# Kernel tuning notes

Hardware: AMD Instinct MI355X
Metric: run time of the kernel (lower is better)

Reference implementation:

```python
import jax, jax.numpy as jnp
import numpy as np
from itertools import product


def _gen_exps(num_vars, degree):
    return [e for e in product(range(degree + 1), repeat=num_vars) if sum(e) <= degree]

EXP_W = _gen_exps(7, 3)  # 120 terms
EXP_B = _gen_exps(3, 3)  # 20 terms
EXP_M = _gen_exps(5, 3)  # 56 terms (+1 diagonal coeff)


def _powers(x, exps):
    return {e: x ** e for e in exps}


def setup_inputs() -> dict:
    key = jax.random.key(0)
    ks = jax.random.split(key, 12)
    B, Din, Dout = 65536, 64, 64
    return {
        'x1': jax.random.normal(ks[0], (B, Din), jnp.float32),
        's1': jax.random.normal(ks[1], (B, Dout), jnp.float32),
        'y1': jax.random.normal(ks[2], (B, Dout), jnp.float32),
        'x2': jax.random.normal(ks[3], (B, Din), jnp.float32),
        's2': jax.random.normal(ks[4], (B, Dout), jnp.float32),
        'y2': jax.random.normal(ks[5], (B, Dout), jnp.float32),
        'w': jax.random.normal(ks[6], (Dout, Din), jnp.float32) * 0.1,
        'b': jax.random.normal(ks[7], (Dout,), jnp.float32) * 0.1,
        'm': jax.random.normal(ks[8], (Dout, Dout), jnp.float32) * 0.1,
        'params_w': jax.random.normal(ks[9], (len(EXP_W),), jnp.float32) * 0.1,
        'params_b': jax.random.normal(ks[10], (len(EXP_B),), jnp.float32) * 0.1,
        'params_m': jax.random.normal(ks[11], (len(EXP_M) + 1,), jnp.float32) * 0.1,
    }


def _dw(x1, s1, y1, x2, s2, y2, w, params_w):
    px1 = _powers(x1, {e[0] for e in EXP_W})
    ps1 = _powers(s1, {e[1] for e in EXP_W})
    py1 = _powers(y1, {e[2] for e in EXP_W})
    px2 = _powers(x2, {e[3] for e in EXP_W})
    ps2 = _powers(s2, {e[4] for e in EXP_W})
    py2 = _powers(y2, {e[5] for e in EXP_W})
    pw = _powers(w, {e[6] for e in EXP_W})
    inv_b = 1.0 / x1.shape[0]
    delta_w = jnp.zeros_like(w)
    for i, e in enumerate(EXP_W):
        y_term = ps1[e[1]] * py1[e[2]] * ps2[e[4]] * py2[e[5]]  # [B, Dout]
        x_term = px1[e[0]] * px2[e[3]]                          # [B, Din]
        delta_w = delta_w + (params_w[i] * inv_b) * (y_term.T @ x_term) * pw[e[6]]
    return delta_w  # bound=None (identity), l2_reg=0


def _db(y1, y2, b, params_b):
    py1 = _powers(y1, {e[0] for e in EXP_B})
    py2 = _powers(y2, {e[1] for e in EXP_B})
    pb = _powers(b, {e[2] for e in EXP_B})
    inv_b = 1.0 / y1.shape[0]
    delta_b = jnp.zeros_like(b)
    for i, e in enumerate(EXP_B):
        delta_b = delta_b + (params_b[i] * inv_b) * jnp.sum(py1[e[0]] * py2[e[1]], axis=0) * pb[e[2]]
    return delta_b


def _dm(y1, y2, m, params_m):
    ey1 = {e[0] for e in EXP_M} | {e[1] for e in EXP_M}
    ey2 = {e[2] for e in EXP_M} | {e[3] for e in EXP_M}
    py1 = _powers(y1, ey1)
    py2 = _powers(y2, ey2)
    pm = _powers(m, {e[4] for e in EXP_M})
    inv_b = 1.0 / y1.shape[0]
    delta_m = jnp.zeros_like(m)
    for i, e in enumerate(EXP_M):
        left = py1[e[1]] * py2[e[3]]   # [B, Dout]
        right = py1[e[0]] * py2[e[2]]  # [B, Dout]
        delta_m = delta_m + (params_m[i] * inv_b) * (left.T @ right) * pm[e[4]]
    delta_m = delta_m + params_m[-1] * jnp.eye(m.shape[0], dtype=m.dtype)
    return delta_m


def reference(x1, s1, y1, x2, s2, y2, w, b, m, params_w, params_b, params_m):
    delta_w = _dw(x1, s1, y1, x2, s2, y2, w, params_w)
    delta_b = _db(y1, y2, b, params_b)
    delta_m = _dm(y1, y2, m, params_m)
    return delta_w, delta_b, delta_m
```

## Files before the change

kernel.cpp:

```cpp
#include <hip/hip_runtime.h>
#include <type_traits>
#include <stdint.h>

#define DEV __device__ __forceinline__

typedef float f32x4 __attribute__((ext_vector_type(4)));
typedef short bf16x8 __attribute__((ext_vector_type(8)));
typedef unsigned short u16;
typedef u16 u16x4 __attribute__((ext_vector_type(4)));

static constexpr int BTOT = 65536;
static constexpr int KB   = 64;
static constexpr int NCHT = BTOT / KB;
static constexpr int NG   = 56;
static constexpr int NCOLSUM = 45;
static constexpr float INVB = 1.0f / (float)BTOT;

static constexpr int NBLK_M  = 24;
static constexpr int NBLK_W1 = 48;
static constexpr int NBLK_W2 = 48;
static constexpr int NBLK_W3 = 64;
static constexpr int NBLK_R  = 328;
static constexpr int GRID    = NBLK_M+NBLK_W1+NBLK_W2+NBLK_W3+NBLK_R;
static constexpr int THR_M  = NBLK_M;
static constexpr int THR_W1 = THR_M + NBLK_W1;
static constexpr int THR_W2 = THR_W1 + NBLK_W2;
static constexpr int THR_W3 = THR_W2 + NBLK_W3;

struct Col {
  int nslot, np, nsplit, nb;
  int8_t sexp[10][6];
  int8_t pa[16], pb[16];
  int16_t gout[16];
  uint8_t ldmask;
};

struct Tables {
  int nW, nB, nM, nA, nX;
  int8_t expw[120][7];
  int8_t expb[20][3];
  int8_t expm[56][5];
  int8_t am[35][4];
  int8_t xm[10][2];
  Col col[4];
  int8_t wtype[120]; int16_t widx[120]; int8_t wpow[120];
  int8_t mtype[56];  int16_t midx[56];  int8_t mpow[56];
  int16_t bcol[20];  int8_t bpow[20];
  int err, gcount;
};

constexpr int aidf(const Tables& t,int a,int b,int c,int d){
  for(int i=0;i<t.nA;i++)
    if(t.am[i][0]==a&&t.am[i][1]==b&&t.am[i][2]==c&&t.am[i][3]==d) return i;
  return -1;
}
constexpr int xidf(const Tables& t,int a,int b){
  for(int i=0;i<t.nX;i++) if(t.xm[i][0]==a&&t.xm[i][1]==b) return i;
  return -1;
}

constexpr Tables makeTables(){
  Tables t{};
  t.err = 0;
  t.nW=0;
  for(int e0=0;e0<4;e0++)for(int e1=0;e1<4;e1++)for(int e2=0;e2<4;e2++)
  for(int e3=0;e3<4;e3++)for(int e4=0;e4<4;e4++)for(int e5=0;e5<4;e5++)
  for(int e6=0;e6<4;e6++) if(e0+e1+e2+e3+e4+e5+e6<=3){
    t.expw[t.nW][0]=(int8_t)e0; t.expw[t.nW][1]=(int8_t)e1; t.expw[t.nW][2]=(int8_t)e2;
    t.expw[t.nW][3]=(int8_t)e3; t.expw[t.nW][4]=(int8_t)e4; t.expw[t.nW][5]=(int8_t)e5;
    t.expw[t.nW][6]=(int8_t)e6; t.nW++;
  }
  t.nB=0;
  for(int e0=0;e0<4;e0++)for(int e1=0;e1<4;e1++)for(int e2=0;e2<4;e2++)
    if(e0+e1+e2<=3){ t.expb[t.nB][0]=(int8_t)e0; t.expb[t.nB][1]=(int8_t)e1; t.expb[t.nB][2]=(int8_t)e2; t.nB++; }
  t.nM=0;
  for(int e0=0;e0<4;e0++)for(int e1=0;e1<4;e1++)for(int e2=0;e2<4;e2++)
  for(int e3=0;e3<4;e3++)for(int e4=0;e4<4;e4++)
    if(e0+e1+e2+e3+e4<=3){
      t.expm[t.nM][0]=(int8_t)e0; t.expm[t.nM][1]=(int8_t)e1; t.expm[t.nM][2]=(int8_t)e2;
      t.expm[t.nM][3]=(int8_t)e3; t.expm[t.nM][4]=(int8_t)e4; t.nM++;
    }
  t.nA=0;
  for(int a=0;a<4;a++)for(int b=0;b<4;b++)for(int c=0;c<4;c++)for(int d=0;d<4;d++)
    if(a+b+c+d<=3){ t.am[t.nA][0]=(int8_t)a; t.am[t.nA][1]=(int8_t)b; t.am[t.nA][2]=(int8_t)c; t.am[t.nA][3]=(int8_t)d; t.nA++; }
  t.nX=0;
  for(int a=0;a<4;a++)for(int b=0;b<4;b++)
    if(a+b<=3){ t.xm[t.nX][0]=(int8_t)a; t.xm[t.nX][1]=(int8_t)b; t.nX++; }

  int wslot[35][10]; int mslot[10][10];
  for(int i=0;i<35;i++)for(int j=0;j<10;j++) wslot[i][j]=-1;
  for(int i=0;i<10;i++)for(int j=0;j<10;j++) mslot[i][j]=-1;

  int slot=0;

  {
    Col& c = t.col[0]; c.nslot=5; c.nsplit=1; c.nb=NBLK_M;
    int ye[5][2] = {{0,1},{1,0},{0,2},{1,1},{2,0}};
    int xmid[5] = {0,0,0,0,0};
    for(int s=0;s<5;s++){
      c.sexp[s][0]=0; c.sexp[s][1]=(int8_t)ye[s][0]; c.sexp[s][2]=0;
      c.sexp[s][3]=(int8_t)ye[s][1]; c.sexp[s][4]=0; c.sexp[s][5]=0;
      xmid[s]=xidf(t, ye[s][0], ye[s][1]);
      if(xmid[s]<0) t.err+=1;
    }
    int p=0;
    for(int L=0;L<2;L++)for(int R=0;R<5;R++){
      c.pa[p]=(int8_t)L; c.pb[p]=(int8_t)R; c.gout[p]=(int16_t)slot;
      mslot[xmid[L]][xmid[R]]=slot; slot++; p++;
    }
    for(int L=2;L<5;L++)for(int R=0;R<2;R++){
      c.pa[p]=(int8_t)L; c.pb[p]=(int8_t)R; c.gout[p]=(int16_t)slot;
      mslot[xmid[L]][xmid[R]]=slot; slot++; p++;
    }
    c.np=p;
    if(p!=16) t.err+=1;
  }
  for(int wc=0; wc<2; wc++){
    Col& c = t.col[1+wc]; c.nslot=10; c.nsplit=1; c.nb = wc? NBLK_W2 : NBLK_W1;
    int ae[5][2] = {{1,0},{0,1},{2,0},{1,1},{0,2}};
    int xe[5][2] = {{0,1},{1,0},{0,2},{1,1},{2,0}};
    int amid[5]={0,0,0,0,0}, xmidb[5]={0,0,0,0,0};
    for(int s=0;s<5;s++){
      for(int q=0;q<6;q++) c.sexp[s][q]=0;
      if(wc==0){ c.sexp[s][0]=(int8_t)ae[s][0]; c.sexp[s][1]=(int8_t)ae[s][1];
                 amid[s]=aidf(t, ae[s][0], ae[s][1], 0, 0); }
      else     { c.sexp[s][2]=(int8_t)ae[s][0]; c.sexp[s][3]=(int8_t)ae[s][1];
                 amid[s]=aidf(t, 0, 0, ae[s][0], ae[s][1]); }
      if(amid[s]<0) t.err+=1;
      for(int q=0;q<6;q++) c.sexp[5+s][q]=0;
      c.sexp[5+s][4]=(int8_t)xe[s][0]; c.sexp[5+s][5]=(int8_t)xe[s][1];
      xmidb[s]=xidf(t, xe[s][0], xe[s][1]);
      if(xmidb[s]<0) t.err+=1;
    }
    int p=0;
    for(int a=0;a<2;a++)for(int b=0;b<5;b++){
      c.pa[p]=(int8_t)a; c.pb[p]=(int8_t)(5+b); c.gout[p]=(int16_t)slot;
      wslot[amid[a]][xmidb[b]]=slot; slot++; p++;
    }
    for(int a=2;a<5;a++)for(int b=0;b<2;b++){
      c.pa[p]=(int8_t)a; c.pb[p]=(int8_t)(5+b); c.gout[p]=(int16_t)slot;
      wslot[amid[a]][xmidb[b]]=slot; slot++; p++;
    }
    c.np=p;
    if(p!=16) t.err+=1;
  }
  {
    Col& c = t.col[3]; c.nslot=6; c.nsplit=2; c.nb=NBLK_W3;
    int ae4[4][4] = {{1,0,1,0},{1,0,0,1},{0,1,1,0},{0,1,0,1}};
    int xe[2][2] = {{0,1},{1,0}};
    int amid[4]={0,0,0,0}, xmidb[2]={0,0};
    for(int s=0;s<4;s++){
      c.sexp[s][0]=(int8_t)ae4[s][0]; c.sexp[s][1]=(int8_t)ae4[s][1];
      c.sexp[s][2]=(int8_t)ae4[s][2]; c.sexp[s][3]=(int8_t)ae4[s][3];
      c.sexp[s][4]=0; c.sexp[s][5]=0;
      amid[s]=aidf(t, ae4[s][0], ae4[s][1], ae4[s][2], ae4[s][3]);
      if(amid[s]<0) t.err+=1;
    }
    for(int s=0;s<2;s++){
      for(int q=0;q<6;q++) c.sexp[4+s][q]=0;
      c.sexp[4+s][4]=(int8_t)xe[s][0]; c.sexp[4+s][5]=(int8_t)xe[s][1];
      xmidb[s]=xidf(t, xe[s][0], xe[s][1]);
      if(xmidb[s]<0) t.err+=1;
    }
    int p=0;
    for(int a=0;a<4;a++)for(int b=0;b<2;b++){
      c.pa[p]=(int8_t)a; c.pb[p]=(int8_t)(4+b); c.gout[p]=(int16_t)slot;
      wslot[amid[a]][xmidb[b]]=slot; slot++; p++;
    }
    c.np=p;
    if(p!=8) t.err+=1;
  }
  t.gcount=slot;
  if(slot!=NG) t.err+=1;

  for(int ci=0; ci<4; ci++){
    unsigned m=0;
    for(int s=0;s<t.col[ci].nslot;s++)
      for(int v=0;v<6;v++) if(t.col[ci].sexp[s][v]>0) m |= (1u<<v);
    t.col[ci].ldmask=(uint8_t)m;
  }

  for(int i=0;i<t.nW;i++){
    const int8_t* e=t.expw[i];
    bool u0=(e[0]==0&&e[3]==0);
    bool v0=(e[1]==0&&e[2]==0&&e[4]==0&&e[5]==0);
    t.wpow[i]=e[6];
    if(u0){ t.wtype[i]=1; t.widx[i]=(int16_t)aidf(t,e[1],e[2],e[4],e[5]); }
    else if(v0){ t.wtype[i]=2; t.widx[i]=(int16_t)xidf(t,e[0],e[3]); }
    else {
      int s=wslot[aidf(t,e[1],e[2],e[4],e[5])][xidf(t,e[0],e[3])];
      if(s<0) t.err+=1;
      t.wtype[i]=0; t.widx[i]=(int16_t)s;
    }
  }
  for(int i=0;i<t.nM;i++){
    const int8_t* e=t.expm[i];
    bool L0=(e[1]==0&&e[3]==0), R0=(e[0]==0&&e[2]==0);
    t.mpow[i]=e[4];
    if(L0){ t.mtype[i]=2; t.midx[i]=(int16_t)aidf(t,0,e[0],0,e[2]); }
    else if(R0){ t.mtype[i]=1; t.midx[i]=(int16_t)aidf(t,0,e[1],0,e[3]); }
    else {
      int s=mslot[xidf(t,e[1],e[3])][xidf(t,e[0],e[2])];
      if(s<0) t.err+=1;
      t.mtype[i]=0; t.midx[i]=(int16_t)s;
    }
  }
  for(int i=0;i<t.nB;i++){
    const int8_t* e=t.expb[i];
    t.bcol[i]=(int16_t)aidf(t,0,e[0],0,e[1]); t.bpow[i]=e[2];
  }
  return t;
}

constexpr Tables TB = makeTables();
static_assert(TB.err==0 && TB.gcount==56, "table build failed");
static_assert(TB.nW==120 && TB.nB==20 && TB.nM==56 && TB.nA==35 && TB.nX==10, "enumeration mismatch");

template<int N, typename F>
DEV void sunroll(F&& f){
  if constexpr (N > 0){
    sunroll<N-1>(static_cast<F&&>(f));
    f(std::integral_constant<int, N-1>{});
  }
}
template<int E> DEV float ipw(float x){
  if constexpr(E==0) return 1.0f;
  else if constexpr(E==1) return x;
  else if constexpr(E==2) return x*x;
  else return x*x*x;
}
DEV u16 f2bf(float f){
  uint32_t u = __builtin_bit_cast(uint32_t, f);
  u = u + 0x7FFFu + ((u>>16)&1u);
  return (u16)(u>>16);
}

DEV bf16x8 readFrag(const u16* lds, int slot, int sb, int t, int l){
  const int base = slot*4096 + ((sb*2 + ((l>>4)>>1))*256 + t*64 + ((l>>4)&1)*32 + (l&15))*4;
  const u16x4 lo = *(const u16x4*)&lds[base];
  const u16x4 hi = *(const u16x4*)&lds[base + 64];
  bf16x8 r;
  r[0]=(short)lo[0]; r[1]=(short)lo[1]; r[2]=(short)lo[2]; r[3]=(short)lo[3];
  r[4]=(short)hi[0]; r[5]=(short)hi[1]; r[6]=(short)hi[2]; r[7]=(short)hi[3];
  return r;
}

template<int CI>
DEV void colGemm(const float* __restrict__ s1,const float* __restrict__ y1,
                 const float* __restrict__ s2,const float* __restrict__ y2,
                 const float* __restrict__ x1,const float* __restrict__ x2,
                 float* __restrict__ G, u16* lds, int tid, int bi)
{
  constexpr int NS  = TB.col[CI].nslot;
  constexpr int NSP = TB.col[CI].nsplit;
  constexpr int NDB = 4/NSP;
  constexpr int NB  = TB.col[CI].nb;
  constexpr unsigned LM = TB.col[CI].ldmask;

  const int l=tid&63, ob=(tid>>6)&3, sub=tid>>8, w=tid>>6;
  const int ch = ob*16 + (l&15);
  const int bl = sub*16 + ((l>>4)&3)*4;

  int aslot=0,bslot=0,gsl=0,dbase=0;
  sunroll<16>([&](auto W){
    constexpr int ww = decltype(W)::value;
    if(w==ww){
      constexpr int p = ww/NSP;
      aslot = TB.col[CI].pa[p];
      bslot = TB.col[CI].pb[p];
      gsl   = TB.col[CI].gout[p];
      dbase = (ww%NSP)*2;
    }
  });

  const int c0 = (bi*NCHT)/NB, c1 = ((bi+1)*NCHT)/NB;
  f32x4 acc[4][NDB] = {};

  float raw[6][4] = {};
  float nraw[6][4] = {};

  auto issue = [&](int ck, float (&dst)[6][4]){
    const int b0 = (ck*KB + bl)*64 + ch;
    #pragma unroll
    for(int j=0;j<4;j++){
      const int off = b0 + j*64;
      if constexpr(LM&1u)  dst[0][j]=s1[off];
      if constexpr(LM&2u)  dst[1][j]=y1[off];
      if constexpr(LM&4u)  dst[2][j]=s2[off];
      if constexpr(LM&8u)  dst[3][j]=y2[off];
      if constexpr(LM&16u) dst[4][j]=x1[off];
      if constexpr(LM&32u) dst[5][j]=x2[off];
    }
  };

  issue(c0, raw);

  for(int ck=c0; ck<c1; ++ck){
    const int nk = (ck+1<c1)? ck+1 : c0;
    issue(nk, nraw);

    sunroll<NS>([&](auto S){
      constexpr int s = decltype(S)::value;
      u16x4 o4;
      #pragma unroll
      for(int j=0;j<4;j++){
        float v = ipw<TB.col[CI].sexp[s][0]>(raw[0][j])
                * ipw<TB.col[CI].sexp[s][1]>(raw[1][j])
                * ipw<TB.col[CI].sexp[s][2]>(raw[2][j])
                * ipw<TB.col[CI].sexp[s][3]>(raw[3][j])
                * ipw<TB.col[CI].sexp[s][4]>(raw[4][j])
                * ipw<TB.col[CI].sexp[s][5]>(raw[5][j]);
        o4[j]=f2bf(v);
      }
      *(u16x4*)&lds[s*4096 + tid*4] = o4;
    });

    asm volatile("s_waitcnt lgkmcnt(0)" ::: "memory");
    __builtin_amdgcn_s_barrier();
    __builtin_amdgcn_sched_barrier(0);

    #pragma unroll
    for(int sb=0; sb<2; ++sb){
      bf16x8 Af[4];
      #pragma unroll
      for(int o2=0;o2<4;o2++) Af[o2]=readFrag(lds,aslot,sb,o2,l);
      #pragma unroll
      for(int dd=0;dd<NDB;dd++){
        bf16x8 Bf=readFrag(lds,bslot,sb,dbase+dd,l);
        #pragma unroll
        for(int o2=0;o2<4;o2++)
          acc[o2][dd]=__builtin_amdgcn_mfma_f32_16x16x32_bf16(Af[o2],Bf,acc[o2][dd],0,0,0);
      }
    }

    __builtin_amdgcn_sched_barrier(0);
    __builtin_amdgcn_s_barrier();
    __builtin_amdgcn_sched_barrier(0);

    #pragma unroll
    for(int a=0;a<6;a++)
      #pragma unroll
      for(int j=0;j<4;j++) raw[a][j]=nraw[a][j];
  }

  float* dst = G + gsl*4096;
  const int r0=(l>>4)*4, cc=l&15;
  #pragma unroll
  for(int o2=0;o2<4;o2++)
    #pragma unroll
    for(int dd=0;dd<NDB;dd++)
      #pragma unroll
      for(int r=0;r<4;r++)
        atomicAdd(&dst[(o2*16+r0+r)*64 + (dbase+dd)*16+cc], acc[o2][dd][r]);
}

DEV void colRed(const float* __restrict__ s1,const float* __restrict__ y1,
                const float* __restrict__ s2,const float* __restrict__ y2,
                const float* __restrict__ x1,const float* __restrict__ x2,
                float* __restrict__ col, float* ldsF, int tid, int bi)
{
  const int ch=tid&63, g=tid>>6;
  const int c0=(bi*NCHT)/NBLK_R, c1=((bi+1)*NCHT)/NBLK_R;
  float accv[45];
  sunroll<45>([&](auto K){ accv[decltype(K)::value]=0.f; });
  for(int r=c0*KB+g; r<c1*KB; r+=16){
    const int off=r*64+ch;
    const float v0=s1[off],v1=y1[off],v2=s2[off],v3=y2[off],v4=x1[off],v5=x2[off];
    sunroll<35>([&](auto K){
      constexpr int k=decltype(K)::value;
      accv[k] += ipw<TB.am[k][0]>(v0)*ipw<TB.am[k][1]>(v1)*ipw<TB.am[k][2]>(v2)*ipw<TB.am[k][3]>(v3);
    });
    sunroll<10>([&](auto K){
      constexpr int k=decltype(K)::value;
      accv[35+k] += ipw<TB.xm[k][0]>(v4)*ipw<TB.xm[k][1]>(v5);
    });
  }
  sunroll<5>([&](auto RR){
    constexpr int rr=decltype(RR)::value;
    __syncthreads();
    sunroll<9>([&](auto Q){
      constexpr int q=decltype(Q)::value;
      ldsF[(q*16+g)*64+ch]=accv[rr*9+q];
    });
    __syncthreads();
    if(tid<576){
      const int q=tid>>6, c=tid&63;
      float s=0.f;
      #pragma unroll
      for(int gg=0; gg<16; gg++) s+=ldsF[(q*16+gg)*64+c];
      atomicAdd(&col[(rr*9+q)*64+c], s);
    }
  });
}

__global__ __launch_bounds__(1024) void k_main(
    const float* __restrict__ x1, const float* __restrict__ s1, const float* __restrict__ y1,
    const float* __restrict__ x2, const float* __restrict__ s2, const float* __restrict__ y2,
    float* __restrict__ G, float* __restrict__ col)
{
  __shared__ u16 lds[10*4096];
  const int tid = threadIdx.x;
  const int bx = blockIdx.x;
  if      (bx < THR_M)  colGemm<0>(s1,y1,s2,y2,x1,x2,G,lds,tid,bx);
  else if (bx < THR_W1) colGemm<1>(s1,y1,s2,y2,x1,x2,G,lds,tid,bx-THR_M);
  else if (bx < THR_W2) colGemm<2>(s1,y1,s2,y2,x1,x2,G,lds,tid,bx-THR_W1);
  else if (bx < THR_W3) colGemm<3>(s1,y1,s2,y2,x1,x2,G,lds,tid,bx-THR_W2);
  else                  colRed(s1,y1,s2,y2,x1,x2,col,(float*)lds,tid,bx-THR_W3);
}

__global__ __launch_bounds__(256) void k_combine(
    const float* __restrict__ G, const float* __restrict__ col,
    const float* __restrict__ w, const float* __restrict__ b, const float* __restrict__ m,
    const float* __restrict__ parw, const float* __restrict__ parb, const float* __restrict__ parm,
    float* __restrict__ out)
{
  const int n = blockIdx.x*256 + threadIdx.x;
  const int o = n>>6, d = n&63;
  const float wv = w[n], mv = m[n];
  const float wp[4] = {1.f, wv, wv*wv, wv*wv*wv};
  const float mp[4] = {1.f, mv, mv*mv, mv*mv*mv};
  float aw=0.f, am=0.f;
  sunroll<120>([&](auto II){
    constexpr int i = decltype(II)::value;
    constexpr int ty = TB.wtype[i];
    constexpr int ix = TB.widx[i];
    constexpr int q  = TB.wpow[i];
    float val;
    if constexpr(ty==0) val = G[ix*4096 + n];
    else if constexpr(ty==1) val = col[ix*64 + o];
    else val = col[(35+ix)*64 + d];
    aw += parw[i] * val * wp[q];
  });
  sunroll<56>([&](auto II){
    constexpr int i = decltype(II)::value;
    constexpr int ty = TB.mtype[i];
    constexpr int ix = TB.midx[i];
    constexpr int q  = TB.mpow[i];
    float val;
    if constexpr(ty==0) val = G[ix*4096 + n];
    else if constexpr(ty==1) val = col[ix*64 + o];
    else val = col[ix*64 + d];
    am += parm[i] * val * mp[q];
  });
  aw *= INVB; am *= INVB;
  if (o==d) am += parm[56];
  out[n] = aw;
  out[4160 + n] = am;
  if (n < 64){
    const float bv = b[n];
    const float bp[4] = {1.f, bv, bv*bv, bv*bv*bv};
    float ab=0.f;
    sunroll<20>([&](auto II){
      constexpr int i = decltype(II)::value;
      constexpr int cix = TB.bcol[i];
      constexpr int q = TB.bpow[i];
      ab += parb[i] * col[cix*64 + n] * bp[q];
    });
    out[4096 + n] = ab * INVB;
  }
}

extern "C" void kernel_launch(void* const* d_in, const int* in_sizes, int n_in,
                              void* d_out, int out_size, void* d_ws, size_t ws_size,
                              hipStream_t stream)
{
  const float* x1=(const float*)d_in[0];
  const float* s1=(const float*)d_in[1];
  const float* y1=(const float*)d_in[2];
  const float* x2=(const float*)d_in[3];
  const float* s2=(const float*)d_in[4];
  const float* y2=(const float*)d_in[5];
  const float* w =(const float*)d_in[6];
  const float* b =(const float*)d_in[7];
  const float* m =(const float*)d_in[8];
  const float* parw=(const float*)d_in[9];
  const float* parb=(const float*)d_in[10];
  const float* parm=(const float*)d_in[11];

  float* G   = (float*)d_ws;
  float* col = G + NG*4096;

  hipMemsetAsync(d_ws, 0, (size_t)(NG*4096 + NCOLSUM*64)*sizeof(float), stream);
  k_main<<<GRID, 1024, 0, stream>>>(x1,s1,y1,x2,s2,y2,G,col);
  k_combine<<<16, 256, 0, stream>>>(G,col,w,b,m,parw,parb,parm,(float*)d_out);
}
```

Before: 103.6 us.

## Store LDS in MFMA fragment order and rebalance grid into uniform windows

Each thread now writes its bf16 values into LDS at positions that already match the MFMA fragment layout. Fragment reads become a single 16-byte load instead of two 8-byte loads plus a repack. The grid is also rebalanced: every GEMM column type gets 64 blocks and the reduction gets 256 blocks, indexed by window. This changes how work is split across CUs and how chunks are spread. The new write pattern may cause LDS bank conflicts on the store side.

```diff
diff --git a/kernel.cpp b/kernel.cpp
--- a/kernel.cpp
+++ b/kernel.cpp
@@ -16,16 +16,10 @@
 static constexpr int NCOLSUM = 45;
 static constexpr float INVB = 1.0f / (float)BTOT;
 
-static constexpr int NBLK_M  = 24;
-static constexpr int NBLK_W1 = 48;
-static constexpr int NBLK_W2 = 48;
-static constexpr int NBLK_W3 = 64;
-static constexpr int NBLK_R  = 328;
-static constexpr int GRID    = NBLK_M+NBLK_W1+NBLK_W2+NBLK_W3+NBLK_R;
-static constexpr int THR_M  = NBLK_M;
-static constexpr int THR_W1 = THR_M + NBLK_W1;
-static constexpr int THR_W2 = THR_W1 + NBLK_W2;
-static constexpr int THR_W3 = THR_W2 + NBLK_W3;
+static constexpr int NWIN   = 64;
+static constexpr int NBLK_C = 64;
+static constexpr int NBLK_R = 256;
+static constexpr int GRID   = 8*NWIN;
 
 struct Col {
   int nslot, np, nsplit, nb;
@@ -94,7 +88,7 @@
   int slot=0;
 
   {
-    Col& c = t.col[0]; c.nslot=5; c.nsplit=1; c.nb=NBLK_M;
+    Col& c = t.col[0]; c.nslot=5; c.nsplit=1; c.nb=NBLK_C;
     int ye[5][2] = {{0,1},{1,0},{0,2},{1,1},{2,0}};
     int xmid[5] = {0,0,0,0,0};
     for(int s=0;s<5;s++){
@@ -116,7 +110,7 @@
     if(p!=16) t.err+=1;
   }
   for(int wc=0; wc<2; wc++){
-    Col& c = t.col[1+wc]; c.nslot=10; c.nsplit=1; c.nb = wc? NBLK_W2 : NBLK_W1;
+    Col& c = t.col[1+wc]; c.nslot=10; c.nsplit=1; c.nb=NBLK_C;
     int ae[5][2] = {{1,0},{0,1},{2,0},{1,1},{0,2}};
     int xe[5][2] = {{0,1},{1,0},{0,2},{1,1},{2,0}};
     int amid[5]={0,0,0,0,0}, xmidb[5]={0,0,0,0,0};
@@ -145,7 +139,7 @@
     if(p!=16) t.err+=1;
   }
   {
-    Col& c = t.col[3]; c.nslot=6; c.nsplit=2; c.nb=NBLK_W3;
+    Col& c = t.col[3]; c.nslot=6; c.nsplit=2; c.nb=NBLK_C;
     int ae4[4][4] = {{1,0,1,0},{1,0,0,1},{0,1,1,0},{0,1,0,1}};
     int xe[2][2] = {{0,1},{1,0}};
     int amid[4]={0,0,0,0}, xmidb[2]={0,0};
@@ -236,13 +230,7 @@
 }
 
 DEV bf16x8 readFrag(const u16* lds, int slot, int sb, int t, int l){
-  const int base = slot*4096 + ((sb*2 + ((l>>4)>>1))*256 + t*64 + ((l>>4)&1)*32 + (l&15))*4;
-  const u16x4 lo = *(const u16x4*)&lds[base];
-  const u16x4 hi = *(const u16x4*)&lds[base + 64];
-  bf16x8 r;
-  r[0]=(short)lo[0]; r[1]=(short)lo[1]; r[2]=(short)lo[2]; r[3]=(short)lo[3];
-  r[4]=(short)hi[0]; r[5]=(short)hi[1]; r[6]=(short)hi[2]; r[7]=(short)hi[3];
-  return r;
+  return *(const bf16x8*)&lds[slot*4096 + ((sb*4 + t)*64 + l)*8];
 }
 
 template<int CI>
@@ -258,8 +246,10 @@
   constexpr unsigned LM = TB.col[CI].ldmask;
 
   const int l=tid&63, ob=(tid>>6)&3, sub=tid>>8, w=tid>>6;
+  const int q = (l>>4)&3;
   const int ch = ob*16 + (l&15);
-  const int bl = sub*16 + ((l>>4)&3)*4;
+  const int bl = sub*16 + q*4;
+  const int wbase = ((( (sub>>1)*4 + ob)*64) + ((sub&1)*2 + (q>>1))*16 + (l&15))*8 + (q&1)*4;
 
   int aslot=0,bslot=0,gsl=0,dbase=0;
   sunroll<16>([&](auto W){
@@ -312,7 +302,7 @@
                 * ipw<TB.col[CI].sexp[s][5]>(raw[5][j]);
         o4[j]=f2bf(v);
       }
-      *(u16x4*)&lds[s*4096 + tid*4] = o4;
+      *(u16x4*)&lds[s*4096 + wbase] = o4;
     });
 
     asm volatile("s_waitcnt lgkmcnt(0)" ::: "memory");
@@ -400,12 +390,13 @@
 {
   __shared__ u16 lds[10*4096];
   const int tid = threadIdx.x;
-  const int bx = blockIdx.x;
-  if      (bx < THR_M)  colGemm<0>(s1,y1,s2,y2,x1,x2,G,lds,tid,bx);
-  else if (bx < THR_W1) colGemm<1>(s1,y1,s2,y2,x1,x2,G,lds,tid,bx-THR_M);
-  else if (bx < THR_W2) colGemm<2>(s1,y1,s2,y2,x1,x2,G,lds,tid,bx-THR_W1);
-  else if (bx < THR_W3) colGemm<3>(s1,y1,s2,y2,x1,x2,G,lds,tid,bx-THR_W2);
-  else                  colRed(s1,y1,s2,y2,x1,x2,col,(float*)lds,tid,bx-THR_W3);
+  const int u = blockIdx.x >> 6;
+  const int g = blockIdx.x & 63;
+  if      (u==0) colGemm<0>(s1,y1,s2,y2,x1,x2,G,lds,tid,g);
+  else if (u==1) colGemm<1>(s1,y1,s2,y2,x1,x2,G,lds,tid,g);
+  else if (u==2) colGemm<2>(s1,y1,s2,y2,x1,x2,G,lds,tid,g);
+  else if (u==3) colGemm<3>(s1,y1,s2,y2,x1,x2,G,lds,tid,g);
+  else           colRed(s1,y1,s2,y2,x1,x2,col,(float*)lds,tid, g*4 + (u-4));
 }
 
 __global__ __launch_bounds__(256) void k_combine(
```

Result: slower. 108.9 us (+5.1%).
